# Performance work log

Hardware: AMD Instinct MI355X
Metric: run time of the kernel (lower is better)

Reference implementation:

```python
import jax, jax.numpy as jnp
import numpy as np
from jax import lax

B, S, D, H, T = 128, 512, 128, 128, 20


def setup_inputs() -> dict:
    key = jax.random.key(0)
    ks = jax.random.split(key, 16)
    sc = 1.0 / np.sqrt(H)
    u = lambda k, shape: jax.random.uniform(k, shape, jnp.float32, -sc, sc)
    return {
        "inputs": jax.random.normal(ks[0], (B, S, D), jnp.float32),
        "tags": jax.random.randint(ks[1], (B, S), 0, T),
        "mask": jnp.ones((B, S), jnp.bool_),
        "w_ih_f": u(ks[2], (4 * H, D)),
        "w_hh_f": u(ks[3], (4 * H, H)),
        "b_f": u(ks[4], (4 * H,)),
        "w_ih_b": u(ks[5], (4 * H, D)),
        "w_hh_b": u(ks[6], (4 * H, H)),
        "b_b": u(ks[7], (4 * H,)),
        "w_out": u(ks[8], (T, 2 * H)),
        "b_out": u(ks[9], (T,)),
        "start_trans": jax.random.uniform(ks[10], (T,), jnp.float32, -0.1, 0.1),
        "end_trans": jax.random.uniform(ks[11], (T,), jnp.float32, -0.1, 0.1),
        "trans": jax.random.uniform(ks[12], (T, T), jnp.float32, -0.1, 0.1),
    }


def _lstm_dir(x, w_ih, w_hh, b, reverse):
    # x: [B,S,D] -> hidden states [B,S,H]
    xp = jnp.einsum('bsd,gd->bsg', x, w_ih) + b  # precomputed input gates [B,S,4H]
    if reverse:
        xp = xp[:, ::-1]
    h0 = jnp.zeros((x.shape[0], H), x.dtype)
    c0 = jnp.zeros((x.shape[0], H), x.dtype)

    def step(carry, xt):
        h, c = carry
        g = xt + h @ w_hh.T
        i, f, gg, o = jnp.split(g, 4, axis=-1)
        i, f, o = jax.nn.sigmoid(i), jax.nn.sigmoid(f), jax.nn.sigmoid(o)
        c = f * c + i * jnp.tanh(gg)
        h = o * jnp.tanh(c)
        return (h, c), h

    _, hs = lax.scan(step, (h0, c0), xp.transpose(1, 0, 2))
    hs = hs.transpose(1, 0, 2)  # [B,S,H]
    if reverse:
        hs = hs[:, ::-1]
    return hs


def _crf_nll(em, tags, mask, start_trans, end_trans, trans):
    # em: [B,S,T]; torchcrf log-likelihood, reduction='mean', negated
    b, s, t = em.shape
    maskf = mask.astype(em.dtype)
    batch = jnp.arange(b)
    # numerator: score of the gold path
    num = start_trans[tags[:, 0]] + em[batch, 0, tags[:, 0]]
    em_tag = jnp.take_along_axis(em, tags[:, :, None], axis=2)[:, :, 0]  # [B,S]
    trans_tag = trans[tags[:, :-1], tags[:, 1:]]  # [B,S-1]
    num = num + jnp.sum((trans_tag + em_tag[:, 1:]) * maskf[:, 1:], axis=1)
    seq_ends = jnp.sum(mask.astype(jnp.int32), axis=1) - 1
    num = num + end_trans[tags[batch, seq_ends]]
    # denominator: forward algorithm (logsumexp semiring) via scan
    score0 = start_trans[None, :] + em[:, 0]  # [B,T]

    def step(score, inp):
        em_t, m_t = inp
        nxt = jax.nn.logsumexp(score[:, :, None] + trans[None] + em_t[:, None, :], axis=1)
        return jnp.where(m_t[:, None], nxt, score), None

    score, _ = lax.scan(step, score0, (em[:, 1:].transpose(1, 0, 2), mask[:, 1:].T))
    den = jax.nn.logsumexp(score + end_trans[None, :], axis=1)
    return -jnp.mean(num - den)


def reference(inputs, tags, mask, w_ih_f, w_hh_f, b_f, w_ih_b, w_hh_b, b_b,
              w_out, b_out, start_trans, end_trans, trans):
    h_f = _lstm_dir(inputs, w_ih_f, w_hh_f, b_f, reverse=False)
    h_b = _lstm_dir(inputs, w_ih_b, w_hh_b, b_b, reverse=True)
    lstm_out = jnp.concatenate([h_f, h_b], axis=-1)  # [B,S,2H]
    emissions = jnp.einsum('bsh,th->bst', lstm_out, w_out) + b_out  # [B,S,T]
    return _crf_nll(emissions, tags, mask, start_trans, end_trans, trans)
```

## Files before the change

kernel.cpp:

```cpp
#include <hip/hip_runtime.h>
#include <cstdint>
#include <cstddef>

#define DEVINL __device__ __forceinline__

constexpr int Bz = 128, Sl = 512, Dm = 128, Hd = 128, NC = 1024, Tt = 20;
constexpr int Mrows = Bz * Sl;

constexpr size_t OFF_WBF  = 0;
constexpr size_t OFF_XP   = 17043456;
constexpr size_t OFF_HS   = 151261184;
constexpr size_t OFF_EM   = 184815616;
constexpr size_t OFF_PART = 190058496;

constexpr float LOG2E  = 1.4426950408889634f;
constexpr float LOG2E2 = 2.8853900817779268f;

DEVINL unsigned short f2bf(float f) {
    uint32_t u = __float_as_uint(f);
    u += 0x7fffu + ((u >> 16) & 1u);
    return (unsigned short)(u >> 16);
}
DEVINL float bf2f(unsigned short h) { return __uint_as_float(((uint32_t)h) << 16); }

DEVINL float rcpf(float x) { return __builtin_amdgcn_rcpf(x); }
DEVINL float exp2f_fast(float x) { return __builtin_amdgcn_exp2f(x); }

DEVINL void barrier_lds_only() {
    __asm__ __volatile__("s_waitcnt lgkmcnt(0)" ::: "memory");
    __builtin_amdgcn_s_barrier();
    __asm__ __volatile__("" ::: "memory");
}

typedef __attribute__((ext_vector_type(8))) __bf16 bf16x8;
typedef __attribute__((ext_vector_type(4))) float f32x4;
typedef _Float16 __attribute__((ext_vector_type(2))) half2_t;
typedef _Float16 __attribute__((ext_vector_type(8))) half8_t;

__global__ __launch_bounds__(256) void wcvt_k(
    const float* __restrict__ wf, const float* __restrict__ wb,
    unsigned short* __restrict__ o)
{
    const int idx = (blockIdx.x * 256 + threadIdx.x) * 4;
    const float* src = (idx < 65536) ? (wf + idx) : (wb + (idx - 65536));
    float4 v = *(const float4*)src;
    ushort4 u; u.x = f2bf(v.x); u.y = f2bf(v.y); u.z = f2bf(v.z); u.w = f2bf(v.w);
    *(ushort4*)(o + idx) = u;
}

__global__ __launch_bounds__(256, 2) void gemm_xp_k(
    const float* __restrict__ X, const unsigned short* __restrict__ wbf,
    const float* __restrict__ b_f, const float* __restrict__ b_b,
    unsigned short* __restrict__ xp)
{
    __shared__ __align__(16) unsigned short As[128 * 132];
    __shared__ __align__(16) unsigned short Bs[128 * 132];
    const int m0 = blockIdx.x * 128;
    const int tid = threadIdx.x;
    const int wave = tid >> 6, lane = tid & 63;
    const int wm = wave * 32;
    const int ln = lane & 15, qd = lane >> 4;
    const int colc = (tid & 31) * 4, rowb = tid >> 5;

    #pragma unroll
    for (int r = 0; r < 16; ++r) {
        int row = rowb + r * 8;
        float4 av = *(const float4*)(&X[(size_t)(m0 + row) * 128 + colc]);
        ushort4 au; au.x = f2bf(av.x); au.y = f2bf(av.y); au.z = f2bf(av.z); au.w = f2bf(av.w);
        *(ushort4*)(&As[row * 132 + colc]) = au;
    }

    const int bidx = m0 >> 9;
    const int tbase = m0 & 511;

    for (int nt = 0; nt < 8; ++nt) {
        const unsigned short* Bsrc = wbf + (size_t)nt * 128 * 128;
        __syncthreads();
        #pragma unroll
        for (int r = 0; r < 16; ++r) {
            int row = rowb + r * 8;
            *(ushort4*)(&Bs[row * 132 + colc]) =
                *(const ushort4*)(&Bsrc[(size_t)row * 128 + colc]);
        }
        __syncthreads();

        f32x4 acc[2][8] = {};
        #pragma unroll
        for (int kk = 0; kk < 4; ++kk) {
            const int kb = kk * 32 + qd * 8;
            bf16x8 af[2], bfr[8];
            #pragma unroll
            for (int i = 0; i < 2; ++i)
                af[i] = *(const bf16x8*)(&As[(wm + i * 16 + ln) * 132 + kb]);
            #pragma unroll
            for (int j = 0; j < 8; ++j)
                bfr[j] = *(const bf16x8*)(&Bs[(j * 16 + ln) * 132 + kb]);
            #pragma unroll
            for (int i = 0; i < 2; ++i)
                #pragma unroll
                for (int j = 0; j < 8; ++j)
                    acc[i][j] = __builtin_amdgcn_mfma_f32_16x16x32_bf16(af[i], bfr[j], acc[i][j], 0, 0, 0);
        }
        #pragma unroll
        for (int j = 0; j < 8; ++j) {
            const int col = nt * 128 + j * 16 + ln;
            const float bv = (col < 512) ? b_f[col] : b_b[col - 512];
            const int gate = (col >> 7) & 3;
            const float sc = (gate == 2) ? LOG2E2 : LOG2E;
            #pragma unroll
            for (int i = 0; i < 2; ++i) {
                const int tloc = tbase + wm + i * 16 + qd * 4;
                ushort4 o;
                o.x = f2bf((acc[i][j][0] + bv) * sc); o.y = f2bf((acc[i][j][1] + bv) * sc);
                o.z = f2bf((acc[i][j][2] + bv) * sc); o.w = f2bf((acc[i][j][3] + bv) * sc);
                *(ushort4*)(xp + ((size_t)bidx * 1024 + col) * 512 + tloc) = o;
            }
        }
    }
}

__global__ __launch_bounds__(512, 1) void lstm_k(
    const float* __restrict__ whf, const float* __restrict__ whb,
    const unsigned short* __restrict__ xp, unsigned short* __restrict__ hs)
{
    __shared__ __align__(16) _Float16 h_buf[2][128];
    const int dir = blockIdx.x >> 7;
    const int b   = blockIdx.x & 127;
    const int tid = threadIdx.x;
    const int lane = tid & 63;
    const int wv   = tid >> 6;
    const int ln   = lane & 15;
    const int qd   = lane >> 4;
    const int u    = wv * 16 + ln;

    const float* wsrc = dir ? whb : whf;
    half8_t wfr[4][4];
    #pragma unroll
    for (int j = 0; j < 4; ++j) {
        const float sc = (j == 2) ? LOG2E2 : LOG2E;
        const float* wrow = wsrc + (size_t)(j * 128 + u) * 128;
        #pragma unroll
        for (int kk = 0; kk < 4; ++kk) {
            float4 v0 = *(const float4*)(wrow + kk * 32 + qd * 8);
            float4 v1 = *(const float4*)(wrow + kk * 32 + qd * 8 + 4);
            half8_t hv;
            hv[0] = (_Float16)(v0.x * sc); hv[1] = (_Float16)(v0.y * sc);
            hv[2] = (_Float16)(v0.z * sc); hv[3] = (_Float16)(v0.w * sc);
            hv[4] = (_Float16)(v1.x * sc); hv[5] = (_Float16)(v1.y * sc);
            hv[6] = (_Float16)(v1.z * sc); hv[7] = (_Float16)(v1.w * sc);
            wfr[j][kk] = hv;
        }
    }

    if (tid < 128) { h_buf[0][tid] = (_Float16)0.f; h_buf[1][tid] = (_Float16)0.f; }
    __syncthreads();

    const unsigned short* xr0 = xp + ((size_t)b * 1024 + (size_t)dir * 512 + u) * 512;
    const unsigned short* xr1 = xr0 + (size_t)128 * 512;
    const unsigned short* xr2 = xr0 + (size_t)256 * 512;
    const unsigned short* xr3 = xr0 + (size_t)384 * 512;

    unsigned short* hptr = hs + (size_t)dir * Mrows * 128 + (size_t)b * Sl * 128 + u
                              + (dir ? (size_t)(Sl - 1) * 128 : 0);
    const int hstep = dir ? -128 : 128;

    float c = 0.f;
    const f32x4 zc = {0.f, 0.f, 0.f, 0.f};
    ushort4 cur0, cur1, cur2, cur3;
    {
        const int o0 = dir ? 508 : 0;
        ushort4 r0 = *(const ushort4*)(xr0 + o0);
        ushort4 r1 = *(const ushort4*)(xr1 + o0);
        ushort4 r2 = *(const ushort4*)(xr2 + o0);
        ushort4 r3 = *(const ushort4*)(xr3 + o0);
        cur0 = dir ? ushort4{r0.w, r0.z, r0.y, r0.x} : r0;
        cur1 = dir ? ushort4{r1.w, r1.z, r1.y, r1.x} : r1;
        cur2 = dir ? ushort4{r2.w, r2.z, r2.y, r2.x} : r2;
        cur3 = dir ? ushort4{r3.w, r3.z, r3.y, r3.x} : r3;
    }

    for (int t = 0; t < Sl; t += 4) {
        #pragma unroll
        for (int j = 0; j < 4; ++j) {
            __asm__ __volatile__(""
                : "+v"(wfr[j][0]), "+v"(wfr[j][1]), "+v"(wfr[j][2]), "+v"(wfr[j][3]));
        }

        const int tn = (t + 4 < Sl) ? (t + 4) : 0;
        const int on = dir ? (508 - tn) : tn;
        ushort4 n0 = *(const ushort4*)(xr0 + on);
        ushort4 n1 = *(const ushort4*)(xr1 + on);
        ushort4 n2 = *(const ushort4*)(xr2 + on);
        ushort4 n3 = *(const ushort4*)(xr3 + on);

        #pragma unroll
        for (int s = 0; s < 4; ++s) {
            const int p = s & 1;
            const half8_t* hb = (const half8_t*)&h_buf[p][0];
            half8_t a0 = hb[qd];
            half8_t a1 = hb[4 + qd];
            half8_t a2 = hb[8 + qd];
            half8_t a3 = hb[12 + qd];

            f32x4 ac0, ac1, ac2, ac3;
            ac0 = __builtin_amdgcn_mfma_f32_16x16x32_f16(a0, wfr[0][0], zc, 0, 0, 0);
            ac1 = __builtin_amdgcn_mfma_f32_16x16x32_f16(a0, wfr[1][0], zc, 0, 0, 0);
            ac2 = __builtin_amdgcn_mfma_f32_16x16x32_f16(a0, wfr[2][0], zc, 0, 0, 0);
            ac3 = __builtin_amdgcn_mfma_f32_16x16x32_f16(a0, wfr[3][0], zc, 0, 0, 0);
            ac0 = __builtin_amdgcn_mfma_f32_16x16x32_f16(a1, wfr[0][1], ac0, 0, 0, 0);
            ac1 = __builtin_amdgcn_mfma_f32_16x16x32_f16(a1, wfr[1][1], ac1, 0, 0, 0);
            ac2 = __builtin_amdgcn_mfma_f32_16x16x32_f16(a1, wfr[2][1], ac2, 0, 0, 0);
            ac3 = __builtin_amdgcn_mfma_f32_16x16x32_f16(a1, wfr[3][1], ac3, 0, 0, 0);
            ac0 = __builtin_amdgcn_mfma_f32_16x16x32_f16(a2, wfr[0][2], ac0, 0, 0, 0);
            ac1 = __builtin_amdgcn_mfma_f32_16x16x32_f16(a2, wfr[1][2], ac1, 0, 0, 0);
            ac2 = __builtin_amdgcn_mfma_f32_16x16x32_f16(a2, wfr[2][2], ac2, 0, 0, 0);
            ac3 = __builtin_amdgcn_mfma_f32_16x16x32_f16(a2, wfr[3][2], ac3, 0, 0, 0);
            ac0 = __builtin_amdgcn_mfma_f32_16x16x32_f16(a3, wfr[0][3], ac0, 0, 0, 0);
            ac1 = __builtin_amdgcn_mfma_f32_16x16x32_f16(a3, wfr[1][3], ac1, 0, 0, 0);
            ac2 = __builtin_amdgcn_mfma_f32_16x16x32_f16(a3, wfr[2][3], ac2, 0, 0, 0);
            ac3 = __builtin_amdgcn_mfma_f32_16x16x32_f16(a3, wfr[3][3], ac3, 0, 0, 0);

            const unsigned short xb0 = (s == 0) ? cur0.x : (s == 1) ? cur0.y : (s == 2) ? cur0.z : cur0.w;
            const unsigned short xb1 = (s == 0) ? cur1.x : (s == 1) ? cur1.y : (s == 2) ? cur1.z : cur1.w;
            const unsigned short xb2 = (s == 0) ? cur2.x : (s == 1) ? cur2.y : (s == 2) ? cur2.z : cur2.w;
            const unsigned short xb3 = (s == 0) ? cur3.x : (s == 1) ? cur3.y : (s == 2) ? cur3.z : cur3.w;

            float t0 = ac0[0] + bf2f(xb0);
            float t1 = ac1[0] + bf2f(xb1);
            float t2 = ac2[0] + bf2f(xb2);
            float t3 = ac3[0] + bf2f(xb3);

            float gi = rcpf(1.f + exp2f_fast(-t0));
            float gf = rcpf(1.f + exp2f_fast(-t1));
            float gg = 2.f * rcpf(1.f + exp2f_fast(-t2)) - 1.f;
            float go = rcpf(1.f + exp2f_fast(-t3));
            c = fmaf(gf, c, gi * gg);
            float th = 1.f - 2.f * rcpf(1.f + exp2f_fast(LOG2E2 * c));
            float h = go * th;

            if (qd == 0) {
                _Float16 hh = (_Float16)h;
                h_buf[1 - p][u] = hh;
                unsigned short hbits; __builtin_memcpy(&hbits, &hh, 2);
                *hptr = hbits;
            }
            hptr += hstep;
            barrier_lds_only();
        }
        cur0 = dir ? ushort4{n0.w, n0.z, n0.y, n0.x} : n0;
        cur1 = dir ? ushort4{n1.w, n1.z, n1.y, n1.x} : n1;
        cur2 = dir ? ushort4{n2.w, n2.z, n2.y, n2.x} : n2;
        cur3 = dir ? ushort4{n3.w, n3.z, n3.y, n3.x} : n3;
    }
}

__global__ __launch_bounds__(320, 1) void emis_k(
    const unsigned short* __restrict__ hs, const float* __restrict__ wout,
    const float* __restrict__ bout, float* __restrict__ em)
{
    __shared__ __align__(16) half2_t wlds[20 * 128];
    const int b  = blockIdx.x >> 2;
    const int qt = blockIdx.x & 3;
    const int tid = threadIdx.x;

    #pragma unroll
    for (int k = 0; k < 8; ++k) {
        int i = tid + k * 320;
        wlds[i] = half2_t{(_Float16)wout[2 * i], (_Float16)wout[2 * i + 1]};
    }
    __syncthreads();

    const int tag  = tid % 20;
    const int copy = tid / 20;
    half2_t wreg[128];
    {
        const uint4* wl4 = (const uint4*)&wlds[tag * 128];
        #pragma unroll
        for (int k = 0; k < 32; ++k) {
            uint4 v = wl4[k];
            __builtin_memcpy(&wreg[4 * k], &v, 16);
        }
    }
    const float bo = bout[tag];
    const unsigned short* hf_base = hs + (size_t)b * Sl * 128;
    const unsigned short* hb_base = hs + (size_t)Mrows * 128 + (size_t)b * Sl * 128;

    #pragma unroll
    for (int i = 0; i < 8; ++i) {
        const int t = qt * 128 + copy + 16 * i;
        const uint4* hf4 = (const uint4*)(hf_base + (size_t)t * 128);
        const uint4* hb4 = (const uint4*)(hb_base + (size_t)t * 128);
        float a0 = bo, a1 = 0.f, a2 = 0.f, a3 = 0.f;
        #pragma unroll
        for (int k = 0; k < 16; ++k) {
            uint4 v = hf4[k];
            half2_t h2[4]; __builtin_memcpy(h2, &v, 16);
            a0 = __builtin_amdgcn_fdot2(wreg[4 * k + 0], h2[0], a0, false);
            a1 = __builtin_amdgcn_fdot2(wreg[4 * k + 1], h2[1], a1, false);
            a2 = __builtin_amdgcn_fdot2(wreg[4 * k + 2], h2[2], a2, false);
            a3 = __builtin_amdgcn_fdot2(wreg[4 * k + 3], h2[3], a3, false);
        }
        #pragma unroll
        for (int k = 0; k < 16; ++k) {
            uint4 v = hb4[k];
            half2_t h2[4]; __builtin_memcpy(h2, &v, 16);
            a0 = __builtin_amdgcn_fdot2(wreg[64 + 4 * k + 0], h2[0], a0, false);
            a1 = __builtin_amdgcn_fdot2(wreg[64 + 4 * k + 1], h2[1], a1, false);
            a2 = __builtin_amdgcn_fdot2(wreg[64 + 4 * k + 2], h2[2], a2, false);
            a3 = __builtin_amdgcn_fdot2(wreg[64 + 4 * k + 3], h2[3], a3, false);
        }
        em[((size_t)b * Sl + t) * Tt + tag] = (a0 + a1) + (a2 + a3);
    }
}

__global__ __launch_bounds__(64) void crf_k(
    const float* __restrict__ em, const int* __restrict__ tags,
    const float* __restrict__ st, const float* __restrict__ et,
    const float* __restrict__ trans, float* __restrict__ part)
{
    const int b = blockIdx.x, lane = threadIdx.x;
    const float* emb = em + (size_t)b * Sl * Tt;
    const int* tg = tags + (size_t)b * Sl;

    float nacc = 0.f;
    for (int t = 1 + lane; t < Sl; t += 64) {
        int tp = tg[t - 1], tc = tg[t];
        nacc += trans[tp * Tt + tc] + emb[t * Tt + tc];
    }
    #pragma unroll
    for (int off = 32; off; off >>= 1) nacc += __shfl_down(nacc, off);

    float Etr[20];
    #pragma unroll
    for (int i = 0; i < 20; ++i)
        Etr[i] = (lane < 20) ? __expf(trans[i * Tt + lane]) : 0.f;

    float C = 0.f;
    float p = (lane < 20) ? __expf(st[lane] + emb[lane]) : 0.f;

    float evr[8];
    #pragma unroll
    for (int s = 0; s < 8; ++s) {
        int tt = 1 + s; tt = tt < Sl ? tt : Sl - 1;
        evr[s] = (lane < 20) ? emb[(size_t)tt * Tt + lane] : 0.f;
    }

    for (int t0 = 1; t0 < Sl; t0 += 8) {
        #pragma unroll
        for (int s = 0; s < 8; ++s) {
            const int t = t0 + s;
            if (t < Sl) {
                float ev = evr[s];
                int tf = t + 8; tf = tf < Sl ? tf : Sl - 1;
                evr[s] = (lane < 20) ? emb[(size_t)tf * Tt + lane] : 0.f;

                float q0 = 0.f, q1 = 0.f, q2 = 0.f, q3 = 0.f;
                #pragma unroll
                for (int i = 0; i < 20; i += 4) {
                    q0 = fmaf(__int_as_float(__builtin_amdgcn_readlane(__float_as_int(p), i + 0)), Etr[i + 0], q0);
                    q1 = fmaf(__int_as_float(__builtin_amdgcn_readlane(__float_as_int(p), i + 1)), Etr[i + 1], q1);
                    q2 = fmaf(__int_as_float(__builtin_amdgcn_readlane(__float_as_int(p), i + 2)), Etr[i + 2], q2);
                    q3 = fmaf(__int_as_float(__builtin_amdgcn_readlane(__float_as_int(p), i + 3)), Etr[i + 3], q3);
                }
                p = ((q0 + q1) + (q2 + q3)) * __expf(ev);
                if ((s & 3) == 3) {
                    float S0 = 0.f, S1 = 0.f, S2 = 0.f, S3 = 0.f;
                    #pragma unroll
                    for (int i = 0; i < 20; i += 4) {
                        S0 += __int_as_float(__builtin_amdgcn_readlane(__float_as_int(p), i + 0));
                        S1 += __int_as_float(__builtin_amdgcn_readlane(__float_as_int(p), i + 1));
                        S2 += __int_as_float(__builtin_amdgcn_readlane(__float_as_int(p), i + 2));
                        S3 += __int_as_float(__builtin_amdgcn_readlane(__float_as_int(p), i + 3));
                    }
                    float Ssum = (S0 + S1) + (S2 + S3);
                    C += __logf(Ssum);
                    p *= rcpf(Ssum);
                }
            }
        }
    }
    float f = (lane < 20) ? p * __expf(et[lane]) : 0.f;
    float S0 = 0.f, S1 = 0.f, S2 = 0.f, S3 = 0.f;
    #pragma unroll
    for (int i = 0; i < 20; i += 4) {
        S0 += __int_as_float(__builtin_amdgcn_readlane(__float_as_int(f), i + 0));
        S1 += __int_as_float(__builtin_amdgcn_readlane(__float_as_int(f), i + 1));
        S2 += __int_as_float(__builtin_amdgcn_readlane(__float_as_int(f), i + 2));
        S3 += __int_as_float(__builtin_amdgcn_readlane(__float_as_int(f), i + 3));
    }
    float den = C + __logf((S0 + S1) + (S2 + S3));
    if (lane == 0)
        part[b] = nacc + st[tg[0]] + emb[tg[0]] + et[tg[Sl - 1]] - den;
}

__global__ void fin_k(const float* __restrict__ part, float* __restrict__ out) {
    int l = threadIdx.x;
    float v = part[l] + part[l + 64];
    #pragma unroll
    for (int off = 32; off; off >>= 1) v += __shfl_xor(v, off);
    if (l == 0) out[0] = -v * (1.f / 128.f);
}

extern "C" void kernel_launch(void* const* d_in, const int* in_sizes, int n_in,
                              void* d_out, int out_size, void* d_ws, size_t ws_size,
                              hipStream_t stream) {
    const float* x      = (const float*)d_in[0];
    const int*   tags   = (const int*)d_in[1];
    const float* w_ih_f = (const float*)d_in[3];
    const float* w_hh_f = (const float*)d_in[4];
    const float* b_f    = (const float*)d_in[5];
    const float* w_ih_b = (const float*)d_in[6];
    const float* w_hh_b = (const float*)d_in[7];
    const float* b_b    = (const float*)d_in[8];
    const float* w_out  = (const float*)d_in[9];
    const float* b_out  = (const float*)d_in[10];
    const float* st     = (const float*)d_in[11];
    const float* et     = (const float*)d_in[12];
    const float* trans  = (const float*)d_in[13];
    float* out = (float*)d_out;

    char* ws = (char*)d_ws;
    unsigned short* wbf  = (unsigned short*)(ws + OFF_WBF);
    unsigned short* xp   = (unsigned short*)(ws + OFF_XP);
    unsigned short* hs   = (unsigned short*)(ws + OFF_HS);
    float*          em   = (float*)(ws + OFF_EM);
    float*          part = (float*)(ws + OFF_PART);

    wcvt_k<<<128, 256, 0, stream>>>(w_ih_f, w_ih_b, wbf);
    gemm_xp_k<<<Mrows / 128, 256, 0, stream>>>(x, wbf, b_f, b_b, xp);
    lstm_k<<<256, 512, 0, stream>>>(w_hh_f, w_hh_b, xp, hs);
    emis_k<<<Bz * 4, 320, 0, stream>>>(hs, w_out, b_out, em);
    crf_k<<<Bz, 64, 0, stream>>>(em, tags, st, et, trans, part);
    fin_k<<<1, 64, 0, stream>>>(part, out);
}
```

Measured before the change: 496.4 us.

## Fuse input-projection GEMM into LSTM kernel with per-chunk LDS staging

Removes the separate gemm_xp kernel and its large bf16 global intermediate. Each LSTM block now computes the input gate projections for 64-timestep chunks using MFMA with register-resident W_ih fragments, then stores them in LDS for the recurrent loop to read. This cuts global memory traffic and one launch. The cost is extra serial work inside the latency-bound recurrence, plus more LDS and registers per block.

Result: faster. 472.4 us (-4.8%).

```diff
diff --git a/kernel.cpp b/kernel.cpp
--- a/kernel.cpp
+++ b/kernel.cpp
@@ -8,7 +8,6 @@
 constexpr int Mrows = Bz * Sl;
 
 constexpr size_t OFF_WBF  = 0;
-constexpr size_t OFF_XP   = 17043456;
 constexpr size_t OFF_HS   = 151261184;
 constexpr size_t OFF_EM   = 184815616;
 constexpr size_t OFF_PART = 190058496;
@@ -48,81 +47,14 @@
     *(ushort4*)(o + idx) = u;
 }
 
-__global__ __launch_bounds__(256, 2) void gemm_xp_k(
+__global__ __launch_bounds__(512, 1) void lstm_k(
     const float* __restrict__ X, const unsigned short* __restrict__ wbf,
     const float* __restrict__ b_f, const float* __restrict__ b_b,
-    unsigned short* __restrict__ xp)
+    const float* __restrict__ whf, const float* __restrict__ whb,
+    unsigned short* __restrict__ hs)
 {
-    __shared__ __align__(16) unsigned short As[128 * 132];
-    __shared__ __align__(16) unsigned short Bs[128 * 132];
-    const int m0 = blockIdx.x * 128;
-    const int tid = threadIdx.x;
-    const int wave = tid >> 6, lane = tid & 63;
-    const int wm = wave * 32;
-    const int ln = lane & 15, qd = lane >> 4;
-    const int colc = (tid & 31) * 4, rowb = tid >> 5;
-
-    #pragma unroll
-    for (int r = 0; r < 16; ++r) {
-        int row = rowb + r * 8;
-        float4 av = *(const float4*)(&X[(size_t)(m0 + row) * 128 + colc]);
-        ushort4 au; au.x = f2bf(av.x); au.y = f2bf(av.y); au.z = f2bf(av.z); au.w = f2bf(av.w);
-        *(ushort4*)(&As[row * 132 + colc]) = au;
-    }
-
-    const int bidx = m0 >> 9;
-    const int tbase = m0 & 511;
-
-    for (int nt = 0; nt < 8; ++nt) {
-        const unsigned short* Bsrc = wbf + (size_t)nt * 128 * 128;
-        __syncthreads();
-        #pragma unroll
-        for (int r = 0; r < 16; ++r) {
-            int row = rowb + r * 8;
-            *(ushort4*)(&Bs[row * 132 + colc]) =
-                *(const ushort4*)(&Bsrc[(size_t)row * 128 + colc]);
-        }
-        __syncthreads();
-
-        f32x4 acc[2][8] = {};
-        #pragma unroll
-        for (int kk = 0; kk < 4; ++kk) {
-            const int kb = kk * 32 + qd * 8;
-            bf16x8 af[2], bfr[8];
-            #pragma unroll
-            for (int i = 0; i < 2; ++i)
-                af[i] = *(const bf16x8*)(&As[(wm + i * 16 + ln) * 132 + kb]);
-            #pragma unroll
-            for (int j = 0; j < 8; ++j)
-                bfr[j] = *(const bf16x8*)(&Bs[(j * 16 + ln) * 132 + kb]);
-            #pragma unroll
-            for (int i = 0; i < 2; ++i)
-                #pragma unroll
-                for (int j = 0; j < 8; ++j)
-                    acc[i][j] = __builtin_amdgcn_mfma_f32_16x16x32_bf16(af[i], bfr[j], acc[i][j], 0, 0, 0);
-        }
-        #pragma unroll
-        for (int j = 0; j < 8; ++j) {
-            const int col = nt * 128 + j * 16 + ln;
-            const float bv = (col < 512) ? b_f[col] : b_b[col - 512];
-            const int gate = (col >> 7) & 3;
-            const float sc = (gate == 2) ? LOG2E2 : LOG2E;
-            #pragma unroll
-            for (int i = 0; i < 2; ++i) {
-                const int tloc = tbase + wm + i * 16 + qd * 4;
-                ushort4 o;
-                o.x = f2bf((acc[i][j][0] + bv) * sc); o.y = f2bf((acc[i][j][1] + bv) * sc);
-                o.z = f2bf((acc[i][j][2] + bv) * sc); o.w = f2bf((acc[i][j][3] + bv) * sc);
-                *(ushort4*)(xp + ((size_t)bidx * 1024 + col) * 512 + tloc) = o;
-            }
-        }
-    }
-}
-
-__global__ __launch_bounds__(512, 1) void lstm_k(
-    const float* __restrict__ whf, const float* __restrict__ whb,
-    const unsigned short* __restrict__ xp, unsigned short* __restrict__ hs)
-{
+    __shared__ __align__(16) unsigned short xl[512 * 72];
+    __shared__ __align__(16) unsigned short Xs[64 * 132];
     __shared__ __align__(16) _Float16 h_buf[2][128];
     const int dir = blockIdx.x >> 7;
     const int b   = blockIdx.x & 127;
@@ -152,13 +84,24 @@
         }
     }
 
+    bf16x8 wih[4][4];
+    #pragma unroll
+    for (int n = 0; n < 4; ++n)
+        #pragma unroll
+        for (int k = 0; k < 4; ++k)
+            wih[n][k] = *(const bf16x8*)&wbf[((size_t)(dir * 512 + wv * 64 + n * 16 + ln)) * 128
+                                            + k * 32 + qd * 8];
+    const float* bsrc = dir ? b_b : b_f;
+    float bvn[4];
+    #pragma unroll
+    for (int n = 0; n < 4; ++n) bvn[n] = bsrc[wv * 64 + n * 16 + ln];
+    const float scw = ((wv >> 1) == 2) ? LOG2E2 : LOG2E;
+
     if (tid < 128) { h_buf[0][tid] = (_Float16)0.f; h_buf[1][tid] = (_Float16)0.f; }
     __syncthreads();
 
-    const unsigned short* xr0 = xp + ((size_t)b * 1024 + (size_t)dir * 512 + u) * 512;
-    const unsigned short* xr1 = xr0 + (size_t)128 * 512;
-    const unsigned short* xr2 = xr0 + (size_t)256 * 512;
-    const unsigned short* xr3 = xr0 + (size_t)384 * 512;
+    const float* Xb = X + (size_t)b * 512 * 128;
+    const int colc = (tid & 31) * 4, rowb = tid >> 5;
 
     unsigned short* hptr = hs + (size_t)dir * Mrows * 128 + (size_t)b * Sl * 128 + u
                               + (dir ? (size_t)(Sl - 1) * 128 : 0);
@@ -166,91 +109,141 @@
 
     float c = 0.f;
     const f32x4 zc = {0.f, 0.f, 0.f, 0.f};
-    ushort4 cur0, cur1, cur2, cur3;
-    {
-        const int o0 = dir ? 508 : 0;
-        ushort4 r0 = *(const ushort4*)(xr0 + o0);
-        ushort4 r1 = *(const ushort4*)(xr1 + o0);
-        ushort4 r2 = *(const ushort4*)(xr2 + o0);
-        ushort4 r3 = *(const ushort4*)(xr3 + o0);
-        cur0 = dir ? ushort4{r0.w, r0.z, r0.y, r0.x} : r0;
-        cur1 = dir ? ushort4{r1.w, r1.z, r1.y, r1.x} : r1;
-        cur2 = dir ? ushort4{r2.w, r2.z, r2.y, r2.x} : r2;
-        cur3 = dir ? ushort4{r3.w, r3.z, r3.y, r3.x} : r3;
-    }
-
-    for (int t = 0; t < Sl; t += 4) {
-        #pragma unroll
-        for (int j = 0; j < 4; ++j) {
-            __asm__ __volatile__(""
-                : "+v"(wfr[j][0]), "+v"(wfr[j][1]), "+v"(wfr[j][2]), "+v"(wfr[j][3]));
-        }
-
-        const int tn = (t + 4 < Sl) ? (t + 4) : 0;
-        const int on = dir ? (508 - tn) : tn;
-        ushort4 n0 = *(const ushort4*)(xr0 + on);
-        ushort4 n1 = *(const ushort4*)(xr1 + on);
-        ushort4 n2 = *(const ushort4*)(xr2 + on);
-        ushort4 n3 = *(const ushort4*)(xr3 + on);
-
-        #pragma unroll
-        for (int s = 0; s < 4; ++s) {
-            const int p = s & 1;
-            const half8_t* hb = (const half8_t*)&h_buf[p][0];
-            half8_t a0 = hb[qd];
-            half8_t a1 = hb[4 + qd];
-            half8_t a2 = hb[8 + qd];
-            half8_t a3 = hb[12 + qd];
-
-            f32x4 ac0, ac1, ac2, ac3;
-            ac0 = __builtin_amdgcn_mfma_f32_16x16x32_f16(a0, wfr[0][0], zc, 0, 0, 0);
-            ac1 = __builtin_amdgcn_mfma_f32_16x16x32_f16(a0, wfr[1][0], zc, 0, 0, 0);
-            ac2 = __builtin_amdgcn_mfma_f32_16x16x32_f16(a0, wfr[2][0], zc, 0, 0, 0);
-            ac3 = __builtin_amdgcn_mfma_f32_16x16x32_f16(a0, wfr[3][0], zc, 0, 0, 0);
-            ac0 = __builtin_amdgcn_mfma_f32_16x16x32_f16(a1, wfr[0][1], ac0, 0, 0, 0);
-            ac1 = __builtin_amdgcn_mfma_f32_16x16x32_f16(a1, wfr[1][1], ac1, 0, 0, 0);
-            ac2 = __builtin_amdgcn_mfma_f32_16x16x32_f16(a1, wfr[2][1], ac2, 0, 0, 0);
-            ac3 = __builtin_amdgcn_mfma_f32_16x16x32_f16(a1, wfr[3][1], ac3, 0, 0, 0);
-            ac0 = __builtin_amdgcn_mfma_f32_16x16x32_f16(a2, wfr[0][2], ac0, 0, 0, 0);
-            ac1 = __builtin_amdgcn_mfma_f32_16x16x32_f16(a2, wfr[1][2], ac1, 0, 0, 0);
-            ac2 = __builtin_amdgcn_mfma_f32_16x16x32_f16(a2, wfr[2][2], ac2, 0, 0, 0);
-            ac3 = __builtin_amdgcn_mfma_f32_16x16x32_f16(a2, wfr[3][2], ac3, 0, 0, 0);
-            ac0 = __builtin_amdgcn_mfma_f32_16x16x32_f16(a3, wfr[0][3], ac0, 0, 0, 0);
-            ac1 = __builtin_amdgcn_mfma_f32_16x16x32_f16(a3, wfr[1][3], ac1, 0, 0, 0);
-            ac2 = __builtin_amdgcn_mfma_f32_16x16x32_f16(a3, wfr[2][3], ac2, 0, 0, 0);
-            ac3 = __builtin_amdgcn_mfma_f32_16x16x32_f16(a3, wfr[3][3], ac3, 0, 0, 0);
-
-            const unsigned short xb0 = (s == 0) ? cur0.x : (s == 1) ? cur0.y : (s == 2) ? cur0.z : cur0.w;
-            const unsigned short xb1 = (s == 0) ? cur1.x : (s == 1) ? cur1.y : (s == 2) ? cur1.z : cur1.w;
-            const unsigned short xb2 = (s == 0) ? cur2.x : (s == 1) ? cur2.y : (s == 2) ? cur2.z : cur2.w;
-            const unsigned short xb3 = (s == 0) ? cur3.x : (s == 1) ? cur3.y : (s == 2) ? cur3.z : cur3.w;
-
-            float t0 = ac0[0] + bf2f(xb0);
-            float t1 = ac1[0] + bf2f(xb1);
-            float t2 = ac2[0] + bf2f(xb2);
-            float t3 = ac3[0] + bf2f(xb3);
-
-            float gi = rcpf(1.f + exp2f_fast(-t0));
-            float gf = rcpf(1.f + exp2f_fast(-t1));
-            float gg = 2.f * rcpf(1.f + exp2f_fast(-t2)) - 1.f;
-            float go = rcpf(1.f + exp2f_fast(-t3));
-            c = fmaf(gf, c, gi * gg);
-            float th = 1.f - 2.f * rcpf(1.f + exp2f_fast(LOG2E2 * c));
-            float h = go * th;
-
-            if (qd == 0) {
-                _Float16 hh = (_Float16)h;
-                h_buf[1 - p][u] = hh;
-                unsigned short hbits; __builtin_memcpy(&hbits, &hh, 2);
-                *hptr = hbits;
+
+    const int r0 = (0 * 128 + u) * 72;
+    const int r1 = (1 * 128 + u) * 72;
+    const int r2 = (2 * 128 + u) * 72;
+    const int r3 = (3 * 128 + u) * 72;
+
+    for (int ch = 0; ch < 8; ++ch) {
+        const int tlo = dir ? (448 - 64 * ch) : (64 * ch);
+
+        #pragma unroll
+        for (int r = 0; r < 4; ++r) {
+            const int row = rowb + r * 16;
+            float4 av = *(const float4*)&Xb[(size_t)(tlo + row) * 128 + colc];
+            ushort4 au; au.x = f2bf(av.x); au.y = f2bf(av.y); au.z = f2bf(av.z); au.w = f2bf(av.w);
+            *(ushort4*)&Xs[row * 132 + colc] = au;
+        }
+        barrier_lds_only();
+
+        {
+            f32x4 acc[4][4];
+            #pragma unroll
+            for (int k = 0; k < 4; ++k) {
+                const int kb = k * 32 + qd * 8;
+                bf16x8 af[4];
+                #pragma unroll
+                for (int m = 0; m < 4; ++m)
+                    af[m] = *(const bf16x8*)&Xs[(m * 16 + ln) * 132 + kb];
+                #pragma unroll
+                for (int m = 0; m < 4; ++m)
+                    #pragma unroll
+                    for (int n = 0; n < 4; ++n)
+                        acc[m][n] = (k == 0)
+                            ? __builtin_amdgcn_mfma_f32_16x16x32_bf16(af[m], wih[n][0], zc, 0, 0, 0)
+                            : __builtin_amdgcn_mfma_f32_16x16x32_bf16(af[m], wih[n][k], acc[m][n], 0, 0, 0);
             }
-            hptr += hstep;
-            barrier_lds_only();
-        }
-        cur0 = dir ? ushort4{n0.w, n0.z, n0.y, n0.x} : n0;
-        cur1 = dir ? ushort4{n1.w, n1.z, n1.y, n1.x} : n1;
-        cur2 = dir ? ushort4{n2.w, n2.z, n2.y, n2.x} : n2;
-        cur3 = dir ? ushort4{n3.w, n3.z, n3.y, n3.x} : n3;
+            #pragma unroll
+            for (int m = 0; m < 4; ++m)
+                #pragma unroll
+                for (int n = 0; n < 4; ++n) {
+                    const int gg = wv * 64 + n * 16 + ln;
+                    ushort4 o;
+                    o.x = f2bf((acc[m][n][0] + bvn[n]) * scw);
+                    o.y = f2bf((acc[m][n][1] + bvn[n]) * scw);
+                    o.z = f2bf((acc[m][n][2] + bvn[n]) * scw);
+                    o.w = f2bf((acc[m][n][3] + bvn[n]) * scw);
+                    *(ushort4*)&xl[gg * 72 + m * 16 + qd * 4] = o;
+                }
+        }
+        barrier_lds_only();
+
+        const int tt0 = dir ? 60 : 0;
+        ushort4 cur0, cur1, cur2, cur3;
+        {
+            ushort4 q0 = *(const ushort4*)&xl[r0 + tt0];
+            ushort4 q1 = *(const ushort4*)&xl[r1 + tt0];
+            ushort4 q2 = *(const ushort4*)&xl[r2 + tt0];
+            ushort4 q3 = *(const ushort4*)&xl[r3 + tt0];
+            cur0 = dir ? ushort4{q0.w, q0.z, q0.y, q0.x} : q0;
+            cur1 = dir ? ushort4{q1.w, q1.z, q1.y, q1.x} : q1;
+            cur2 = dir ? ushort4{q2.w, q2.z, q2.y, q2.x} : q2;
+            cur3 = dir ? ushort4{q3.w, q3.z, q3.y, q3.x} : q3;
+        }
+
+        for (int gi = 0; gi < 16; ++gi) {
+            #pragma unroll
+            for (int j = 0; j < 4; ++j) {
+                __asm__ __volatile__(""
+                    : "+v"(wfr[j][0]), "+v"(wfr[j][1]), "+v"(wfr[j][2]), "+v"(wfr[j][3]));
+            }
+            int ttn = dir ? (56 - gi * 4) : (gi * 4 + 4);
+            if (ttn < 0) ttn = 0;
+            ushort4 n0 = *(const ushort4*)&xl[r0 + ttn];
+            ushort4 n1 = *(const ushort4*)&xl[r1 + ttn];
+            ushort4 n2 = *(const ushort4*)&xl[r2 + ttn];
+            ushort4 n3 = *(const ushort4*)&xl[r3 + ttn];
+
+            #pragma unroll
+            for (int s = 0; s < 4; ++s) {
+                const int p = s & 1;
+                const half8_t* hb = (const half8_t*)&h_buf[p][0];
+                half8_t a0 = hb[qd];
+                half8_t a1 = hb[4 + qd];
+                half8_t a2 = hb[8 + qd];
+                half8_t a3 = hb[12 + qd];
+
+                f32x4 ac0, ac1, ac2, ac3;
+                ac0 = __builtin_amdgcn_mfma_f32_16x16x32_f16(a0, wfr[0][0], zc, 0, 0, 0);
+                ac1 = __builtin_amdgcn_mfma_f32_16x16x32_f16(a0, wfr[1][0], zc, 0, 0, 0);
+                ac2 = __builtin_amdgcn_mfma_f32_16x16x32_f16(a0, wfr[2][0], zc, 0, 0, 0);
+                ac3 = __builtin_amdgcn_mfma_f32_16x16x32_f16(a0, wfr[3][0], zc, 0, 0, 0);
+                ac0 = __builtin_amdgcn_mfma_f32_16x16x32_f16(a1, wfr[0][1], ac0, 0, 0, 0);
+                ac1 = __builtin_amdgcn_mfma_f32_16x16x32_f16(a1, wfr[1][1], ac1, 0, 0, 0);
+                ac2 = __builtin_amdgcn_mfma_f32_16x16x32_f16(a1, wfr[2][1], ac2, 0, 0, 0);
+                ac3 = __builtin_amdgcn_mfma_f32_16x16x32_f16(a1, wfr[3][1], ac3, 0, 0, 0);
+                ac0 = __builtin_amdgcn_mfma_f32_16x16x32_f16(a2, wfr[0][2], ac0, 0, 0, 0);
+                ac1 = __builtin_amdgcn_mfma_f32_16x16x32_f16(a2, wfr[1][2], ac1, 0, 0, 0);
+                ac2 = __builtin_amdgcn_mfma_f32_16x16x32_f16(a2, wfr[2][2], ac2, 0, 0, 0);
+                ac3 = __builtin_amdgcn_mfma_f32_16x16x32_f16(a2, wfr[3][2], ac3, 0, 0, 0);
+                ac0 = __builtin_amdgcn_mfma_f32_16x16x32_f16(a3, wfr[0][3], ac0, 0, 0, 0);
+                ac1 = __builtin_amdgcn_mfma_f32_16x16x32_f16(a3, wfr[1][3], ac1, 0, 0, 0);
+                ac2 = __builtin_amdgcn_mfma_f32_16x16x32_f16(a3, wfr[2][3], ac2, 0, 0, 0);
+                ac3 = __builtin_amdgcn_mfma_f32_16x16x32_f16(a3, wfr[3][3], ac3, 0, 0, 0);
+
+                const unsigned short xb0 = (s == 0) ? cur0.x : (s == 1) ? cur0.y : (s == 2) ? cur0.z : cur0.w;
+                const unsigned short xb1 = (s == 0) ? cur1.x : (s == 1) ? cur1.y : (s == 2) ? cur1.z : cur1.w;
+                const unsigned short xb2 = (s == 0) ? cur2.x : (s == 1) ? cur2.y : (s == 2) ? cur2.z : cur2.w;
+                const unsigned short xb3 = (s == 0) ? cur3.x : (s == 1) ? cur3.y : (s == 2) ? cur3.z : cur3.w;
+
+                float t0 = ac0[0] + bf2f(xb0);
+                float t1 = ac1[0] + bf2f(xb1);
+                float t2 = ac2[0] + bf2f(xb2);
+                float t3 = ac3[0] + bf2f(xb3);
+
+                float gi_ = rcpf(1.f + exp2f_fast(-t0));
+                float gf_ = rcpf(1.f + exp2f_fast(-t1));
+                float gg_ = 2.f * rcpf(1.f + exp2f_fast(-t2)) - 1.f;
+                float go_ = rcpf(1.f + exp2f_fast(-t3));
+                c = fmaf(gf_, c, gi_ * gg_);
+                float th = 1.f - 2.f * rcpf(1.f + exp2f_fast(LOG2E2 * c));
+                float h = go_ * th;
+
+                if (qd == 0) {
+                    _Float16 hh = (_Float16)h;
+                    h_buf[1 - p][u] = hh;
+                    unsigned short hbits; __builtin_memcpy(&hbits, &hh, 2);
+                    *hptr = hbits;
+                }
+                hptr += hstep;
+                barrier_lds_only();
+            }
+            cur0 = dir ? ushort4{n0.w, n0.z, n0.y, n0.x} : n0;
+            cur1 = dir ? ushort4{n1.w, n1.z, n1.y, n1.x} : n1;
+            cur2 = dir ? ushort4{n2.w, n2.z, n2.y, n2.x} : n2;
+            cur3 = dir ? ushort4{n3.w, n3.z, n3.y, n3.x} : n3;
+        }
     }
 }
 
@@ -421,14 +414,12 @@
 
     char* ws = (char*)d_ws;
     unsigned short* wbf  = (unsigned short*)(ws + OFF_WBF);
-    unsigned short* xp   = (unsigned short*)(ws + OFF_XP);
     unsigned short* hs   = (unsigned short*)(ws + OFF_HS);
     float*          em   = (float*)(ws + OFF_EM);
     float*          part = (float*)(ws + OFF_PART);
 
     wcvt_k<<<128, 256, 0, stream>>>(w_ih_f, w_ih_b, wbf);
-    gemm_xp_k<<<Mrows / 128, 256, 0, stream>>>(x, wbf, b_f, b_b, xp);
-    lstm_k<<<256, 512, 0, stream>>>(w_hh_f, w_hh_b, xp, hs);
+    lstm_k<<<256, 512, 0, stream>>>(x, wbf, b_f, b_b, w_hh_f, w_hh_b, hs);
     emis_k<<<Bz * 4, 320, 0, stream>>>(hs, w_out, b_out, em);
     crf_k<<<Bz, 64, 0, stream>>>(em, tags, st, et, trans, part);
     fin_k<<<1, 64, 0, stream>>>(part, out);
```
